# Kernel optimization log

Hardware: AMD Instinct MI355X
Metric: run time of the kernel (lower is better)

Reference implementation:

```python
import jax, jax.numpy as jnp
import numpy as np

B, T, XS, HS = 256, 512, 256, 256


def setup_inputs() -> dict:
    key = jax.random.key(0)
    ks = jax.random.split(key, 9)
    scale_x = np.sqrt(6.0 / (XS + HS)).astype(np.float32)  # xavier_uniform-like scale
    scale_h = np.sqrt(6.0 / (HS + HS)).astype(np.float32)
    d = {"x": jax.random.normal(ks[0], (B, T, XS), dtype=jnp.float32)}
    names = ["i", "f", "g", "o"]
    for n, kx, kh in zip(names, ks[1:5], ks[5:9]):
        d[f"wx_{n}"] = jax.random.uniform(kx, (XS, HS), jnp.float32, -scale_x, scale_x)
        d[f"wh_{n}"] = jax.random.uniform(kh, (HS, HS), jnp.float32, -scale_h, scale_h)
        d[f"bx_{n}"] = jnp.zeros((HS,), jnp.float32)
        d[f"bh_{n}"] = jnp.zeros((HS,), jnp.float32)
    return d


def reference(x, wx_i, bx_i, wh_i, bh_i, wx_f, bx_f, wh_f, bh_f,
              wx_g, bx_g, wh_g, bh_g, wx_o, bx_o, wh_o, bh_o):
    bs, ts, xs = x.shape
    hs = wx_i.shape[1]
    # Fuse the 4 input projections and 4 hidden projections into 2 GEMMs
    # (identical math to 8 separate matmuls).
    Wx = jnp.concatenate([wx_i, wx_f, wx_g, wx_o], axis=1)      # [xs, 4hs]
    Wh = jnp.concatenate([wh_i, wh_f, wh_g, wh_o], axis=1)      # [hs, 4hs]
    b = jnp.concatenate([bx_i + bh_i, bx_f + bh_f, bx_g + bh_g, bx_o + bh_o])

    # Precompute all input projections in one big GEMM: [bs, ts, 4hs]
    x_proj = jnp.einsum('btx,xg->btg', x, Wx) + b

    def step(carry, xt_proj):
        h, c = carry
        gates = xt_proj + h @ Wh                      # [bs, 4hs]
        i_t = jax.nn.sigmoid(gates[:, 0 * hs:1 * hs])
        f_t = jax.nn.sigmoid(gates[:, 1 * hs:2 * hs])
        g_t = jnp.tanh(gates[:, 2 * hs:3 * hs])
        o_t = jax.nn.sigmoid(gates[:, 3 * hs:4 * hs])
        c_new = f_t * c + i_t * g_t
        h_new = o_t * jnp.tanh(c_new)
        return (h_new, c_new), None

    h0 = jnp.zeros((bs, hs), x.dtype)
    c0 = jnp.zeros((bs, hs), x.dtype)
    (h_t, c_t), _ = jax.lax.scan(step, (h0, c0), jnp.swapaxes(x_proj, 0, 1))
    return (h_t, c_t)
```

## Files before the change

kernel.cpp:

```cpp
#include <hip/hip_runtime.h>
#include <hip/hip_bf16.h>

#define BB   256
#define TT   512
#define XSZ  256
#define HSZ  256

typedef __bf16 bf16_t;
typedef __attribute__((ext_vector_type(8))) __bf16 bf16x8;
typedef __attribute__((ext_vector_type(4))) float  f32x4;
typedef __attribute__((ext_vector_type(4))) unsigned uint4v;

__device__ __forceinline__ f32x4 splat4(float v) { f32x4 r = {v, v, v, v}; return r; }

__global__ void prep_bias(const float* bx0, const float* bh0, const float* bx1, const float* bh1,
                          const float* bx2, const float* bh2, const float* bx3, const float* bh3,
                          float* bias) {
  const float* bxs[4] = {bx0, bx1, bx2, bx3};
  const float* bhs[4] = {bh0, bh1, bh2, bh3};
  int g = blockIdx.x, c = threadIdx.x;
  bias[g * 256 + c] = bxs[g][c] + bhs[g][c];
}

__global__ void prep_wtf(const float* wx0, const float* wh0, const float* wx1, const float* wh1,
                         const float* wx2, const float* wh2, const float* wx3, const float* wh3,
                         bf16_t* Wtf) {
  const float* whs[4] = {wh0, wh1, wh2, wh3};
  const float* wxs[4] = {wx0, wx1, wx2, wx3};
  int id  = blockIdx.x * 256 + threadIdx.x;
  int L   = id & 63;
  int kts = (id >> 6) & 15;
  int w   = (id >> 10) & 7;
  int j   = (id >> 13) & 7;
  int tc   = L & 15;
  int gate = tc & 3;
  int hc   = j * 32 + w * 4 + (tc >> 2);
  int k0   = kts * 32 + (L >> 4) * 8;
  const float* src = (k0 < 256) ? (whs[gate] + (size_t)k0 * 256 + hc)
                                : (wxs[gate] + (size_t)(k0 - 256) * 256 + hc);
  bf16x8 v;
#pragma unroll
  for (int i = 0; i < 8; ++i) v[i] = (__bf16)src[(size_t)i * 256];
  reinterpret_cast<bf16x8*>(Wtf)[id] = v;
}

__global__ void prep_xbf(const float* __restrict__ x, bf16_t* __restrict__ xb) {
  size_t id = (size_t)blockIdx.x * 256 + threadIdx.x;
  const float* p = x + id * 8;
  f32x4 lo = *reinterpret_cast<const f32x4*>(p);
  f32x4 hi = *reinterpret_cast<const f32x4*>(p + 4);
  bf16x8 v;
#pragma unroll
  for (int i = 0; i < 4; ++i) { v[i] = (__bf16)lo[i]; v[i + 4] = (__bf16)hi[i]; }
  reinterpret_cast<bf16x8*>(xb)[id] = v;
}

template <bool XBF>
__global__ __launch_bounds__(512, 2)
void lstm_seq(const void* __restrict__ xsrc, const bf16_t* __restrict__ Wtf,
              const float* __restrict__ bias, unsigned* __restrict__ hseq,
              float* __restrict__ out)
{
  __shared__ __align__(16) char bxlds[65536];
  __shared__ __align__(16) char hxl[2][8192];

  const int tid  = threadIdx.x;
  const int w    = tid >> 6;
  const int lane = tid & 63;
  const int l15  = lane & 15, l4 = lane >> 4;
  const int bid  = blockIdx.x;
  const int g    = bid >> 3, j = bid & 7;
  const int b0   = g * 16;
  const int gate = l15 & 3;
  const int hcg  = l15 >> 2;
  const bool isg = (gate == 2);

  const float*  xf32 = (const float*)xsrc;
  const bf16_t* xbf  = (const bf16_t*)xsrc;

  const char* wbase = (const char*)Wtf + ((size_t)(j * 8 + w) * 16) * 1024 + lane * 16;
  bf16x8 Bh[8];
#pragma unroll
  for (int kt = 0; kt < 8; ++kt)
    Bh[kt] = *reinterpret_cast<const bf16x8*>(wbase + kt * 1024);
#pragma unroll
  for (int q = 0; q < 8; ++q) {
    bf16x8 v = *reinterpret_cast<const bf16x8*>(wbase + (8 + q) * 1024);
    *reinterpret_cast<bf16x8*>(bxlds + (w * 8 + q) * 1024 + lane * 16) = v;
  }

  const float bias_v = bias[gate * 256 + j * 32 + w * 4 + hcg];

  f32x4 cst = {0.f, 0.f, 0.f, 0.f};

  __syncthreads();

  f32x4 axa = splat4(bias_v);
  f32x4 axb = {0.f, 0.f, 0.f, 0.f};
#pragma unroll
  for (int k8 = 0; k8 < 8; ++k8) {
    bf16x8 a;
    if constexpr (XBF) {
      a = *reinterpret_cast<const bf16x8*>(
          xbf + (size_t)(b0 + l15) * (TT * XSZ) + k8 * 32 + l4 * 8);
    } else {
      const float* xp = xf32 + (size_t)(b0 + l15) * (TT * XSZ) + k8 * 32 + l4 * 8;
      f32x4 lo = *reinterpret_cast<const f32x4*>(xp);
      f32x4 hi = *reinterpret_cast<const f32x4*>(xp + 4);
#pragma unroll
      for (int i = 0; i < 4; ++i) { a[i] = (__bf16)lo[i]; a[i + 4] = (__bf16)hi[i]; }
    }
    bf16x8 bx = *reinterpret_cast<const bf16x8*>(bxlds + (w * 8 + k8) * 1024 + lane * 16);
    if (k8 & 1) axb = __builtin_amdgcn_mfma_f32_16x16x32_bf16(a, bx, axb, 0, 0, 0);
    else        axa = __builtin_amdgcn_mfma_f32_16x16x32_bf16(a, bx, axa, 0, 0, 0);
  }

#pragma unroll 1
  for (int t = 0; t < TT; ++t) {
    f32x4 acc_a = axa;
    f32x4 acc_b = axb;

    if (t > 0) {
      const unsigned* hp = hseq + (size_t)(t & 1) * 65536
                         + (size_t)(b0 + l15) * HSZ + w * 32 + l4 * 8;
      const unsigned tg = (unsigned)t;
      uint4v A, B;
      for (;;) {
        asm volatile("global_load_dwordx4 %0, %2, off sc0 sc1\n\t"
                     "global_load_dwordx4 %1, %2, off offset:16 sc0 sc1\n\t"
                     "s_waitcnt vmcnt(0)"
                     : "=&v"(A), "=&v"(B) : "v"(hp) : "memory");
        bool ok = ((A[0] >> 16) == tg) & ((A[1] >> 16) == tg) &
                  ((A[2] >> 16) == tg) & ((A[3] >> 16) == tg) &
                  ((B[0] >> 16) == tg) & ((B[1] >> 16) == tg) &
                  ((B[2] >> 16) == tg) & ((B[3] >> 16) == tg);
        if (__all((int)ok)) break;
        __builtin_amdgcn_s_sleep(1);
      }
      __builtin_amdgcn_sched_barrier(0);
      unsigned p0 = (A[0] & 0xFFFFu) | (A[1] << 16);
      unsigned p1 = (A[2] & 0xFFFFu) | (A[3] << 16);
      unsigned p2 = (B[0] & 0xFFFFu) | (B[1] << 16);
      unsigned p3 = (B[2] & 0xFFFFu) | (B[3] << 16);
      uint4v pk = {p0, p1, p2, p3};
      *reinterpret_cast<uint4v*>(hxl[t & 1] + w * 1024 + lane * 16) = pk;
    }
    __syncthreads();

    if (t > 0) {
#pragma unroll
      for (int kt = 0; kt < 8; ++kt) {
        bf16x8 a = *reinterpret_cast<const bf16x8*>(hxl[t & 1] + kt * 1024 + lane * 16);
        if (kt & 1) acc_b = __builtin_amdgcn_mfma_f32_16x16x32_bf16(a, Bh[kt], acc_b, 0, 0, 0);
        else        acc_a = __builtin_amdgcn_mfma_f32_16x16x32_bf16(a, Bh[kt], acc_a, 0, 0, 0);
      }
    }

    f32x4 av;
#pragma unroll
    for (int r = 0; r < 4; ++r) {
      float vr = acc_a[r] + acc_b[r];
      float p  = isg ? 2.f * vr : vr;
      float s  = 1.f / (1.f + __expf(-p));
      av[r] = isg ? (2.f * s - 1.f) : s;
    }
    f32x4 bv, v0, v1, c0, c1;
#pragma unroll
    for (int r = 0; r < 4; ++r) bv[r] = __shfl_xor(av[r], 1);
#pragma unroll
    for (int r = 0; r < 4; ++r) {
      v0[r] = (gate & 1) ? bv[r] : av[r];
      v1[r] = (gate & 1) ? av[r] : bv[r];
    }
#pragma unroll
    for (int r = 0; r < 4; ++r) { c0[r] = __shfl_xor(v0[r], 2); c1[r] = __shfl_xor(v1[r], 2); }
    f32x4 hv;
#pragma unroll
    for (int r = 0; r < 4; ++r) {
      float iv = (gate & 2) ? c0[r] : v0[r];
      float fv = (gate & 2) ? c1[r] : v1[r];
      float gv = (gate & 2) ? v0[r] : c0[r];
      float ov = (gate & 2) ? v1[r] : c1[r];
      float cn = fv * cst[r] + iv * gv;
      cst[r] = cn;
      float s2 = 1.f / (1.f + __expf(-2.f * cn));
      hv[r] = ov * (2.f * s2 - 1.f);
    }
    float hsel = (gate == 0) ? hv[0] : (gate == 1) ? hv[1] : (gate == 2) ? hv[2] : hv[3];
    float csel = (gate == 0) ? cst[0] : (gate == 1) ? cst[1] : (gate == 2) ? cst[2] : cst[3];

    if (t + 1 < TT) {
      __bf16 hb16 = (__bf16)hsel;
      unsigned hvd = ((unsigned)(t + 1) << 16)
                   | (unsigned)__builtin_bit_cast(unsigned short, hb16);
      unsigned* hp2 = hseq + (size_t)((t + 1) & 1) * 65536
                    + (size_t)(b0 + l4 * 4 + gate) * HSZ + (j * 32 + w * 4 + hcg);
      asm volatile("global_store_dword %0, %1, off sc0 sc1" :: "v"(hp2), "v"(hvd) : "memory");

      axa = splat4(bias_v);
      axb = f32x4{0.f, 0.f, 0.f, 0.f};
#pragma unroll
      for (int k8 = 0; k8 < 8; ++k8) {
        bf16x8 a;
        if constexpr (XBF) {
          a = *reinterpret_cast<const bf16x8*>(
              xbf + (size_t)(b0 + l15) * (TT * XSZ) + (size_t)(t + 1) * XSZ + k8 * 32 + l4 * 8);
        } else {
          const float* xp = xf32 + (size_t)(b0 + l15) * (TT * XSZ)
                          + (size_t)(t + 1) * XSZ + k8 * 32 + l4 * 8;
          f32x4 lo = *reinterpret_cast<const f32x4*>(xp);
          f32x4 hi = *reinterpret_cast<const f32x4*>(xp + 4);
#pragma unroll
          for (int i = 0; i < 4; ++i) { a[i] = (__bf16)lo[i]; a[i + 4] = (__bf16)hi[i]; }
        }
        bf16x8 bx = *reinterpret_cast<const bf16x8*>(bxlds + (w * 8 + k8) * 1024 + lane * 16);
        if (k8 & 1) axb = __builtin_amdgcn_mfma_f32_16x16x32_bf16(a, bx, axb, 0, 0, 0);
        else        axa = __builtin_amdgcn_mfma_f32_16x16x32_bf16(a, bx, axa, 0, 0, 0);
      }
    } else {
      float* op = out + (size_t)(b0 + l4 * 4 + gate) * HSZ + (j * 32 + w * 4 + hcg);
      op[0] = hsel;
      op[(size_t)BB * HSZ] = csel;
    }
  }
}

extern "C" void kernel_launch(void* const* d_in, const int* in_sizes, int n_in,
                              void* d_out, int out_size, void* d_ws, size_t ws_size,
                              hipStream_t stream) {
  const float* x = (const float*)d_in[0];
  const float *wx[4], *wh[4], *bx[4], *bh[4];
  for (int g = 0; g < 4; ++g) {
    wx[g] = (const float*)d_in[1 + 4 * g];
    wh[g] = (const float*)d_in[2 + 4 * g];
    bx[g] = (const float*)d_in[3 + 4 * g];
    bh[g] = (const float*)d_in[4 + 4 * g];
  }

  char* ws = (char*)d_ws;
  float*    bias = (float*)ws;
  bf16_t*   Wtf  = (bf16_t*)(ws + 4096);
  unsigned* hseq = (unsigned*)(ws + 4096 + 1048576);
  bf16_t*   xbf  = (bf16_t*)(ws + 4096 + 1048576 + 524288);
  const size_t need_xbf = 4096 + 1048576 + 524288 + (size_t)BB * TT * XSZ * 2;

  prep_bias<<<dim3(4), dim3(256), 0, stream>>>(bx[0], bh[0], bx[1], bh[1],
                                               bx[2], bh[2], bx[3], bh[3], bias);
  prep_wtf<<<dim3(256), dim3(256), 0, stream>>>(wx[0], wh[0], wx[1], wh[1],
                                                wx[2], wh[2], wx[3], wh[3], Wtf);
  if (ws_size >= need_xbf) {
    prep_xbf<<<dim3((BB * TT * XSZ / 8) / 256), dim3(256), 0, stream>>>(x, xbf);
    lstm_seq<true><<<dim3(128), dim3(512), 0, stream>>>(xbf, Wtf, bias, hseq,
                                                        (float*)d_out);
  } else {
    lstm_seq<false><<<dim3(128), dim3(512), 0, stream>>>(x, Wtf, bias, hseq,
                                                         (float*)d_out);
  }
}
```

Before: 1.877 ms.

## Prefetch next-step hidden state speculatively, drop spin sleep, remap block indices

Result: slower. 2.815 ms (+50.0%).

```diff
diff --git a/kernel.cpp b/kernel.cpp
--- a/kernel.cpp
+++ b/kernel.cpp
@@ -69,7 +69,7 @@
   const int lane = tid & 63;
   const int l15  = lane & 15, l4 = lane >> 4;
   const int bid  = blockIdx.x;
-  const int g    = bid >> 3, j = bid & 7;
+  const int g    = bid & 15, j = bid >> 4;
   const int b0   = g * 16;
   const int gate = l15 & 3;
   const int hcg  = l15 >> 2;
@@ -92,6 +92,7 @@
   const float bias_v = bias[gate * 256 + j * 32 + w * 4 + hcg];
 
   f32x4 cst = {0.f, 0.f, 0.f, 0.f};
+  uint4v pA = {0, 0, 0, 0}, pB = {0, 0, 0, 0};
 
   __syncthreads();
 
@@ -121,27 +122,27 @@
     f32x4 acc_b = axb;
 
     if (t > 0) {
+      const unsigned tg = (unsigned)t;
       const unsigned* hp = hseq + (size_t)(t & 1) * 65536
                          + (size_t)(b0 + l15) * HSZ + w * 32 + l4 * 8;
-      const unsigned tg = (unsigned)t;
-      uint4v A, B;
+      asm volatile("s_waitcnt vmcnt(0)" ::: "memory");
+      __builtin_amdgcn_sched_barrier(0);
       for (;;) {
+        bool ok = ((pA[0] >> 16) == tg) & ((pA[1] >> 16) == tg) &
+                  ((pA[2] >> 16) == tg) & ((pA[3] >> 16) == tg) &
+                  ((pB[0] >> 16) == tg) & ((pB[1] >> 16) == tg) &
+                  ((pB[2] >> 16) == tg) & ((pB[3] >> 16) == tg);
+        if (__all((int)ok)) break;
         asm volatile("global_load_dwordx4 %0, %2, off sc0 sc1\n\t"
                      "global_load_dwordx4 %1, %2, off offset:16 sc0 sc1\n\t"
                      "s_waitcnt vmcnt(0)"
-                     : "=&v"(A), "=&v"(B) : "v"(hp) : "memory");
-        bool ok = ((A[0] >> 16) == tg) & ((A[1] >> 16) == tg) &
-                  ((A[2] >> 16) == tg) & ((A[3] >> 16) == tg) &
-                  ((B[0] >> 16) == tg) & ((B[1] >> 16) == tg) &
-                  ((B[2] >> 16) == tg) & ((B[3] >> 16) == tg);
-        if (__all((int)ok)) break;
-        __builtin_amdgcn_s_sleep(1);
+                     : "=&v"(pA), "=&v"(pB) : "v"(hp) : "memory");
+        __builtin_amdgcn_sched_barrier(0);
       }
-      __builtin_amdgcn_sched_barrier(0);
-      unsigned p0 = (A[0] & 0xFFFFu) | (A[1] << 16);
-      unsigned p1 = (A[2] & 0xFFFFu) | (A[3] << 16);
-      unsigned p2 = (B[0] & 0xFFFFu) | (B[1] << 16);
-      unsigned p3 = (B[2] & 0xFFFFu) | (B[3] << 16);
+      unsigned p0 = (pA[0] & 0xFFFFu) | (pA[1] << 16);
+      unsigned p1 = (pA[2] & 0xFFFFu) | (pA[3] << 16);
+      unsigned p2 = (pB[0] & 0xFFFFu) | (pB[1] << 16);
+      unsigned p3 = (pB[2] & 0xFFFFu) | (pB[3] << 16);
       uint4v pk = {p0, p1, p2, p3};
       *reinterpret_cast<uint4v*>(hxl[t & 1] + w * 1024 + lane * 16) = pk;
     }
@@ -196,6 +197,12 @@
       unsigned* hp2 = hseq + (size_t)((t + 1) & 1) * 65536
                     + (size_t)(b0 + l4 * 4 + gate) * HSZ + (j * 32 + w * 4 + hcg);
       asm volatile("global_store_dword %0, %1, off sc0 sc1" :: "v"(hp2), "v"(hvd) : "memory");
+
+      const unsigned* hpn = hseq + (size_t)((t + 1) & 1) * 65536
+                          + (size_t)(b0 + l15) * HSZ + w * 32 + l4 * 8;
+      asm volatile("global_load_dwordx4 %0, %2, off sc0 sc1\n\t"
+                   "global_load_dwordx4 %1, %2, off offset:16 sc0 sc1"
+                   : "=&v"(pA), "=&v"(pB) : "v"(hpn) : "memory");
 
       axa = splat4(bias_v);
       axb = f32x4{0.f, 0.f, 0.f, 0.f};
```
